# Kernel tuning notes

Hardware: AMD Instinct MI355X
Metric: run time of the kernel (lower is better)

## Reference

```python
import jax, jax.numpy as jnp
import numpy as np

DIMS, K_SIZE, V_SIZE = 256, 64, 64
B, T = 4, 4096


def setup_inputs() -> dict:
    key = jax.random.key(0)
    k1, k2, k3, k4 = jax.random.split(key, 4)
    # glorot-uniform-style init for the projection weights
    def glorot(k, fan_in, fan_out):
        lim = jnp.sqrt(6.0 / (fan_in + fan_out))
        return jax.random.uniform(k, (fan_in, fan_out), jnp.float32, -lim, lim)
    return {
        "inputs": jax.random.normal(k1, (B, T, DIMS), jnp.float32),
        "key_w": glorot(k2, DIMS, K_SIZE),
        "query_w": glorot(k3, DIMS, K_SIZE),
        "value_w": glorot(k4, DIMS, V_SIZE),
    }


def reference(inputs, key_w, query_w, value_w):
    # QKV projections: [B,T,D] @ [D,k] -> [B,T,k]
    keys = jnp.einsum('btd,dk->btk', inputs, key_w)
    queries = jnp.einsum('btd,dk->btk', inputs, query_w)
    values = jnp.einsum('btd,dv->btv', inputs, value_w)
    # full causal score matrix [B,T,T] (faithful to explicit triu mask)
    logits = jnp.einsum('bqk,bsk->bqs', queries, keys)
    q_idx = jnp.arange(logits.shape[1])[:, None]
    s_idx = jnp.arange(logits.shape[2])[None, :]
    causal = s_idx <= q_idx  # lower-triangular incl. diagonal
    sqrt_k = jnp.sqrt(jnp.asarray(key_w.shape[1], jnp.float32))
    masked = jnp.where(causal[None], logits, -jnp.inf)
    probs = jax.nn.softmax(masked / sqrt_k, axis=2)
    read = jnp.einsum('bqs,bsv->bqv', probs, values)
    return jnp.concatenate([inputs, read], axis=-1)  # [B,T,D+V]
```

## Files before the change

kernel.cpp:

```cpp
#include <hip/hip_runtime.h>

#define DIMS 256
#define HK 64
#define NB 4
#define NT 4096
#define BT (NB * NT)

typedef unsigned short u16;
typedef unsigned int u32;

using f32x4  = __attribute__((ext_vector_type(4))) float;
using bf16x8 = __attribute__((ext_vector_type(8))) short;

__device__ __forceinline__ u16 f2bf(float f) {
    u32 u = __float_as_uint(f);
    u = (u + 0x7FFFu + ((u >> 16) & 1u)) >> 16;
    return (u16)u;
}
__device__ __forceinline__ u32 pack2(float a, float b) {
    return (u32)f2bf(a) | ((u32)f2bf(b) << 16);
}
__device__ __forceinline__ float bf2f(short h) {
    return __uint_as_float(((u32)(u16)h) << 16);
}
__device__ __forceinline__ bf16x8 ldb8(const u16* p) {
    return *reinterpret_cast<const bf16x8*>(p);
}
__device__ __forceinline__ u32 cvtpk(float a, float b) {
    u32 r;
    asm("v_cvt_pk_bf16_f32 %0, %1, %2" : "=v"(r) : "v"(a), "v"(b));
    return r;
}
__device__ __forceinline__ bf16x8 cvt8(const float* p) {
    f32x4 a = *reinterpret_cast<const f32x4*>(p);
    f32x4 b = *reinterpret_cast<const f32x4*>(p + 4);
    union { u32 w[4]; bf16x8 v; } u;
    u.w[0] = pack2(a[0], a[1]); u.w[1] = pack2(a[2], a[3]);
    u.w[2] = pack2(b[0], b[1]); u.w[3] = pack2(b[2], b[3]);
    return u.v;
}

__global__ __launch_bounds__(256) void prep_kernel(
    const float* __restrict__ wk, const float* __restrict__ wq,
    const float* __restrict__ wv, u16* __restrict__ Wt)
{
    const int i = (int)(blockIdx.x * 256 + threadIdx.x);
    const int e0 = i * 4;
    const int m = e0 >> 14;
    const int r = e0 & 16383;
    const int col = r >> 8;
    const int k = r & 255;
    const float* w = (m == 0) ? wk : (m == 1) ? wq : wv;
    u32 w0 = pack2(w[(k + 0) * HK + col], w[(k + 1) * HK + col]);
    u32 w1 = pack2(w[(k + 2) * HK + col], w[(k + 3) * HK + col]);
    u32* p = reinterpret_cast<u32*>(Wt + e0);
    p[0] = w0; p[1] = w1;
}

__global__ __launch_bounds__(64) void proj_kernel(
    const float* __restrict__ x, const u16* __restrict__ Wt,
    float* __restrict__ out,
    u16* __restrict__ Qb, u16* __restrict__ Kb, u16* __restrict__ Vt)
{
    const int l = (int)threadIdx.x;
    const int lo = l & 15;
    const int g = l >> 4;
    const int q0 = (int)blockIdx.x * 16;

    const f32x4* x4 = reinterpret_cast<const f32x4*>(x);
    f32x4* out4 = reinterpret_cast<f32x4*>(out);
    #pragma unroll
    for (int c = 0; c < 16; ++c) {
        f32x4 v = x4[(size_t)(q0 + c) * 64 + l];
        out4[(size_t)(q0 + c) * 80 + l] = v;
    }

    bf16x8 a[8];
    #pragma unroll
    for (int kf = 0; kf < 8; ++kf)
        a[kf] = cvt8(x + (size_t)(q0 + lo) * DIMS + kf * 32 + g * 8);

    #pragma unroll
    for (int m = 0; m < 3; ++m) {
        const u16* wb = Wt + m * (HK * DIMS);
        f32x4 acc[4];
        #pragma unroll
        for (int c = 0; c < 4; ++c) acc[c] = f32x4{0.f, 0.f, 0.f, 0.f};

        __builtin_amdgcn_s_setprio(1);
        #pragma unroll
        for (int c = 0; c < 4; ++c) {
            #pragma unroll
            for (int kf = 0; kf < 8; ++kf) {
                bf16x8 bf = ldb8(wb + (size_t)(16 * c + lo) * DIMS + kf * 32 + g * 8);
                acc[c] = __builtin_amdgcn_mfma_f32_16x16x32_bf16(a[kf], bf, acc[c], 0, 0, 0);
            }
        }
        __builtin_amdgcn_s_setprio(0);

        if (m == 2) {
            #pragma unroll
            for (int c = 0; c < 4; ++c)
                #pragma unroll
                for (int ii = 0; ii < 4; ++ii) {
                    const int grow = q0 + 4 * g + ii;
                    Vt[(size_t)((grow >> 12) * HK + 16 * c + lo) * NT + (grow & (NT - 1))] =
                        f2bf(acc[c][ii]);
                }
        } else {
            const float sc = (m == 1) ? 0.125f * 1.44269504f : 1.0f;
            u16* dst = (m == 1) ? Qb : Kb;
            #pragma unroll
            for (int c = 0; c < 4; ++c)
                #pragma unroll
                for (int ii = 0; ii < 4; ++ii)
                    dst[(size_t)(q0 + 4 * g + ii) * HK + 16 * c + lo] = f2bf(acc[c][ii] * sc);
        }
    }
}

template<bool MASK>
__device__ __forceinline__ void qk32(
    const u16* __restrict__ Kb_b, int s0, int q0,
    const bf16x8 (&qf)[2][2], float (&pls)[2], bf16x8 (&pa)[2],
    int lo, int g)
{
    bf16x8 kk[2][2];
    #pragma unroll
    for (int kh = 0; kh < 2; ++kh)
        #pragma unroll
        for (int kf = 0; kf < 2; ++kf)
            kk[kh][kf] = ldb8(Kb_b + (size_t)(s0 + 16 * kh + lo) * HK + kf * 32 + g * 8);

    const f32x4 c28 = f32x4{-28.f, -28.f, -28.f, -28.f};
    f32x4 sv[2][2];
    __builtin_amdgcn_s_setprio(1);
    #pragma unroll
    for (int rh = 0; rh < 2; ++rh)
        #pragma unroll
        for (int kh = 0; kh < 2; ++kh) {
            sv[rh][kh] = __builtin_amdgcn_mfma_f32_16x16x32_bf16(kk[kh][0], qf[rh][0], c28, 0, 0, 0);
            sv[rh][kh] = __builtin_amdgcn_mfma_f32_16x16x32_bf16(kk[kh][1], qf[rh][1], sv[rh][kh], 0, 0, 0);
        }
    __builtin_amdgcn_s_setprio(0);

    #pragma unroll
    for (int rh = 0; rh < 2; ++rh) {
        float p0[4], p1[4];
        #pragma unroll
        for (int ii = 0; ii < 4; ++ii) {
            float v0 = sv[rh][0][ii];
            float v1 = sv[rh][1][ii];
            if (MASK) {
                const int qr = q0 + 16 * rh + lo;
                if (s0 + 4 * g + ii > qr)      v0 = -1e30f;
                if (s0 + 16 + 4 * g + ii > qr) v1 = -1e30f;
            }
            p0[ii] = __builtin_amdgcn_exp2f(v0);
            p1[ii] = __builtin_amdgcn_exp2f(v1);
            pls[rh] += p0[ii] + p1[ii];
        }
        u32 a0 = cvtpk(p0[0], p0[1]), a1 = cvtpk(p0[2], p0[3]);
        u32 b0 = cvtpk(p1[0], p1[1]), b1 = cvtpk(p1[2], p1[3]);
        asm("v_permlane32_swap_b32 %0, %1" : "+v"(a0), "+v"(b0));
        asm("v_permlane16_swap_b32 %0, %1" : "+v"(a0), "+v"(b0));
        asm("v_permlane32_swap_b32 %0, %1" : "+v"(a1), "+v"(b1));
        asm("v_permlane16_swap_b32 %0, %1" : "+v"(a1), "+v"(b1));
        union { u32 w[4]; bf16x8 v; } u;
        u.w[0] = a0; u.w[1] = a1; u.w[2] = b0; u.w[3] = b1;
        pa[rh] = u.v;
    }
}

template<int NK, bool MASK>
__device__ __forceinline__ void body(
    const u16* __restrict__ Kb_b, const u16* __restrict__ Vb, int s0,
    const bf16x8 (&qf)[2][2], float (&pls)[2], f32x4 (&o)[2][4],
    int lo, int g, int q0)
{
    bf16x8 vf[NK][4];
    #pragma unroll
    for (int kf = 0; kf < NK; ++kf)
        #pragma unroll
        for (int c = 0; c < 4; ++c)
            vf[kf][c] = ldb8(Vb + (size_t)(16 * c + lo) * NT + s0 + kf * 32 + g * 8);

    #pragma unroll
    for (int t = 0; t < NK; ++t) {
        bf16x8 pa[2];
        qk32<MASK>(Kb_b, s0 + t * 32, q0, qf, pls, pa, lo, g);
        __builtin_amdgcn_s_setprio(1);
        #pragma unroll
        for (int rh = 0; rh < 2; ++rh)
            #pragma unroll
            for (int c = 0; c < 4; ++c)
                o[rh][c] = __builtin_amdgcn_mfma_f32_16x16x32_bf16(pa[rh], vf[t][c], o[rh][c], 0, 0, 0);
        __builtin_amdgcn_s_setprio(0);
    }
}

__global__ __launch_bounds__(64) void attn_kernel(
    const u16* __restrict__ Qb, const u16* __restrict__ Kb,
    const u16* __restrict__ Vt, u16* __restrict__ Opb, float* __restrict__ lp,
    const int S)
{
    const int l = (int)threadIdx.x;
    const int lo = l & 15;
    const int g = l >> 4;

    const int bid = (int)blockIdx.x;
    const int per = 4 * S;
    const int j = 127 - bid / per;
    const int r = bid % per;
    const int b = r / S;
    const int s = r % S;

    const int q0 = j * 32;
    const int nkv = j + 1;
    const int it0 = (s * nkv) / S;
    const int it1 = ((s + 1) * nkv) / S;

    const u16* Kb_b = Kb + (size_t)b * NT * HK;
    const u16* Vb = Vt + (size_t)b * HK * NT;

    bf16x8 qf[2][2];
    #pragma unroll
    for (int rh = 0; rh < 2; ++rh)
        #pragma unroll
        for (int kf = 0; kf < 2; ++kf)
            qf[rh][kf] = ldb8(Qb + (size_t)(b * NT + q0 + 16 * rh + lo) * HK + kf * 32 + g * 8);

    f32x4 o[2][4];
    float pls[2] = {0.f, 0.f};
    #pragma unroll
    for (int rh = 0; rh < 2; ++rh)
        #pragma unroll
        for (int c = 0; c < 4; ++c) o[rh][c] = f32x4{0.f, 0.f, 0.f, 0.f};

    int it = it0;
    const int itE = (s == S - 1) ? it1 - 1 : it1;
    for (; it + 1 < itE; it += 2)
        body<2, false>(Kb_b, Vb, it * 32, qf, pls, o, lo, g, q0);
    if (it < itE)
        body<1, false>(Kb_b, Vb, it * 32, qf, pls, o, lo, g, q0);
    if (s == S - 1)
        body<1, true>(Kb_b, Vb, (nkv - 1) * 32, qf, pls, o, lo, g, q0);

    const size_t rowbase = (size_t)s * BT + (size_t)b * NT + q0;
    #pragma unroll
    for (int rh = 0; rh < 2; ++rh) {
        #pragma unroll
        for (int c = 0; c < 4; ++c)
            #pragma unroll
            for (int ii = 0; ii < 4; ++ii)
                Opb[(rowbase + 16 * rh + 4 * g + ii) * HK + 16 * c + lo] = f2bf(o[rh][c][ii]);
        float sum = pls[rh];
        sum += __shfl_xor(sum, 16);
        sum += __shfl_xor(sum, 32);
        if (l < 16) lp[rowbase + 16 * rh + lo] = sum;
    }
}

__global__ __launch_bounds__(256) void merge_kernel(
    const u16* __restrict__ Opb, const float* __restrict__ lp,
    float* __restrict__ out, const int S)
{
    const int idx = (int)(blockIdx.x * 256 + threadIdx.x);
    const int row = idx >> 3;
    const int c8 = (idx & 7) * 8;

    float li = 0.f;
    for (int s = 0; s < S; ++s) li += lp[(size_t)s * BT + row];

    float acc[8];
    #pragma unroll
    for (int k = 0; k < 8; ++k) acc[k] = 0.f;
    for (int s = 0; s < S; ++s) {
        bf16x8 v = ldb8(Opb + ((size_t)s * BT + row) * HK + c8);
        #pragma unroll
        for (int k = 0; k < 8; ++k) acc[k] += bf2f(v[k]);
    }
    const float inv = 1.0f / li;
    f32x4 r0 = f32x4{acc[0] * inv, acc[1] * inv, acc[2] * inv, acc[3] * inv};
    f32x4 r1 = f32x4{acc[4] * inv, acc[5] * inv, acc[6] * inv, acc[7] * inv};
    f32x4* dst = reinterpret_cast<f32x4*>(out + (size_t)row * 320 + 256 + c8);
    dst[0] = r0;
    dst[1] = r1;
}

extern "C" void kernel_launch(void* const* d_in, const int* in_sizes, int n_in,
                              void* d_out, int out_size, void* d_ws, size_t ws_size,
                              hipStream_t stream) {
    (void)in_sizes; (void)n_in; (void)out_size;
    const float* x  = (const float*)d_in[0];
    const float* wk = (const float*)d_in[1];
    const float* wq = (const float*)d_in[2];
    const float* wv = (const float*)d_in[3];
    float* out = (float*)d_out;

    char* ws = (char*)d_ws;
    u16* Qb  = (u16*)(ws);
    u16* Kb  = (u16*)(ws + ((size_t)2 << 20));
    u16* Vt  = (u16*)(ws + ((size_t)4 << 20));
    u16* Wt  = (u16*)(ws + ((size_t)6 << 20));
    float* lp = (float*)(ws + ((size_t)6 << 20) + (128 << 10));
    u16* Opb = (u16*)(ws + ((size_t)7 << 20));

    int S = 8;
    while (S > 1 && ((size_t)7 << 20) + (size_t)S * BT * HK * 2 > ws_size) S >>= 1;

    prep_kernel<<<48, 256, 0, stream>>>(wk, wq, wv, Wt);
    proj_kernel<<<BT / 16, 64, 0, stream>>>(x, Wt, out, Qb, Kb, Vt);
    attn_kernel<<<128 * 4 * S, 64, 0, stream>>>(Qb, Kb, Vt, Opb, lp, S);
    merge_kernel<<<512, 256, 0, stream>>>(Opb, lp, out, S);
}
```

Baseline: 77.06 us.

## Double-buffer K/V register loads to prefetch next 32-key tile during compute

Replaces the unrolled two-tile body with a software-pipelined loop that loads the next 32-key K and V fragments into an alternate register buffer while the current tile's QK, exp and PV MFMAs run. The causal mask becomes a runtime flag checked per tile instead of a separate template instantiation. This aims to hide global load latency for a single-wave block, at the cost of more live registers and a runtime branch in the mask path.

```diff
diff --git a/kernel.cpp b/kernel.cpp
--- a/kernel.cpp
+++ b/kernel.cpp
@@ -119,19 +119,26 @@
     }
 }
 
-template<bool MASK>
-__device__ __forceinline__ void qk32(
-    const u16* __restrict__ Kb_b, int s0, int q0,
-    const bf16x8 (&qf)[2][2], float (&pls)[2], bf16x8 (&pa)[2],
-    int lo, int g)
-{
-    bf16x8 kk[2][2];
+__device__ __forceinline__ void ld32(
+    const u16* __restrict__ Kb_b, const u16* __restrict__ Vb, int s0,
+    bf16x8 (&kk)[2][2], bf16x8 (&vf)[4], int lo, int g)
+{
     #pragma unroll
     for (int kh = 0; kh < 2; ++kh)
         #pragma unroll
         for (int kf = 0; kf < 2; ++kf)
             kk[kh][kf] = ldb8(Kb_b + (size_t)(s0 + 16 * kh + lo) * HK + kf * 32 + g * 8);
-
+    #pragma unroll
+    for (int c = 0; c < 4; ++c)
+        vf[c] = ldb8(Vb + (size_t)(16 * c + lo) * NT + s0 + g * 8);
+}
+
+__device__ __forceinline__ void comp32(
+    const bf16x8 (&kk)[2][2], const bf16x8 (&vf)[4],
+    int s0, int q0, bool domask,
+    const bf16x8 (&qf)[2][2], float (&pls)[2], f32x4 (&o)[2][4],
+    int lo, int g)
+{
     const f32x4 c28 = f32x4{-28.f, -28.f, -28.f, -28.f};
     f32x4 sv[2][2];
     __builtin_amdgcn_s_setprio(1);
@@ -151,7 +158,7 @@
         for (int ii = 0; ii < 4; ++ii) {
             float v0 = sv[rh][0][ii];
             float v1 = sv[rh][1][ii];
-            if (MASK) {
+            if (domask) {
                 const int qr = q0 + 16 * rh + lo;
                 if (s0 + 4 * g + ii > qr)      v0 = -1e30f;
                 if (s0 + 16 + 4 * g + ii > qr) v1 = -1e30f;
@@ -168,33 +175,11 @@
         asm("v_permlane16_swap_b32 %0, %1" : "+v"(a1), "+v"(b1));
         union { u32 w[4]; bf16x8 v; } u;
         u.w[0] = a0; u.w[1] = a1; u.w[2] = b0; u.w[3] = b1;
-        pa[rh] = u.v;
-    }
-}
-
-template<int NK, bool MASK>
-__device__ __forceinline__ void body(
-    const u16* __restrict__ Kb_b, const u16* __restrict__ Vb, int s0,
-    const bf16x8 (&qf)[2][2], float (&pls)[2], f32x4 (&o)[2][4],
-    int lo, int g, int q0)
-{
-    bf16x8 vf[NK][4];
-    #pragma unroll
-    for (int kf = 0; kf < NK; ++kf)
+        const bf16x8 pa = u.v;
+        __builtin_amdgcn_s_setprio(1);
         #pragma unroll
         for (int c = 0; c < 4; ++c)
-            vf[kf][c] = ldb8(Vb + (size_t)(16 * c + lo) * NT + s0 + kf * 32 + g * 8);
-
-    #pragma unroll
-    for (int t = 0; t < NK; ++t) {
-        bf16x8 pa[2];
-        qk32<MASK>(Kb_b, s0 + t * 32, q0, qf, pls, pa, lo, g);
-        __builtin_amdgcn_s_setprio(1);
-        #pragma unroll
-        for (int rh = 0; rh < 2; ++rh)
-            #pragma unroll
-            for (int c = 0; c < 4; ++c)
-                o[rh][c] = __builtin_amdgcn_mfma_f32_16x16x32_bf16(pa[rh], vf[t][c], o[rh][c], 0, 0, 0);
+            o[rh][c] = __builtin_amdgcn_mfma_f32_16x16x32_bf16(pa, vf[c], o[rh][c], 0, 0, 0);
         __builtin_amdgcn_s_setprio(0);
     }
 }
@@ -237,14 +222,21 @@
         #pragma unroll
         for (int c = 0; c < 4; ++c) o[rh][c] = f32x4{0.f, 0.f, 0.f, 0.f};
 
+    bf16x8 kkA[2][2], vfA[4], kkB[2][2], vfB[4];
     int it = it0;
-    const int itE = (s == S - 1) ? it1 - 1 : it1;
-    for (; it + 1 < itE; it += 2)
-        body<2, false>(Kb_b, Vb, it * 32, qf, pls, o, lo, g, q0);
-    if (it < itE)
-        body<1, false>(Kb_b, Vb, it * 32, qf, pls, o, lo, g, q0);
-    if (s == S - 1)
-        body<1, true>(Kb_b, Vb, (nkv - 1) * 32, qf, pls, o, lo, g, q0);
+    if (it < it1) {
+        ld32(Kb_b, Vb, it * 32, kkA, vfA, lo, g);
+        while (true) {
+            if (it + 1 < it1) ld32(Kb_b, Vb, (it + 1) * 32, kkB, vfB, lo, g);
+            comp32(kkA, vfA, it * 32, q0, it == nkv - 1, qf, pls, o, lo, g);
+            ++it;
+            if (it >= it1) break;
+            if (it + 1 < it1) ld32(Kb_b, Vb, (it + 1) * 32, kkA, vfA, lo, g);
+            comp32(kkB, vfB, it * 32, q0, it == nkv - 1, qf, pls, o, lo, g);
+            ++it;
+            if (it >= it1) break;
+        }
+    }
 
     const size_t rowbase = (size_t)s * BT + (size_t)b * NT + q0;
     #pragma unroll
```

New measurement: 75.36 us. -2.2%, faster.
